# Optimization experiments

Measured on AMD Instinct MI355X. Metric: run time of the kernel, lower is better.

## Reference

```python
import jax, jax.numpy as jnp
import numpy as np

NUM_TREES = 256
DEPTH = 6
TREE_DIM = 2
INPUT_DIM = 256
BATCH = 2048


def sparsemax(x, axis=0):
    # Euclidean projection onto the simplex along `axis`.
    x = jnp.moveaxis(x, axis, -1)
    z = jnp.flip(jnp.sort(x, axis=-1), axis=-1)           # descending
    cz = jnp.cumsum(z, axis=-1)
    k = jnp.arange(1, x.shape[-1] + 1, dtype=x.dtype)
    support = (1.0 + k * z) > cz                          # boolean support set
    k_sel = jnp.sum(support, axis=-1, keepdims=True)      # |S(z)|
    tau = (jnp.take_along_axis(cz, k_sel - 1, axis=-1) - 1.0) / k_sel.astype(x.dtype)
    out = jnp.maximum(x - tau, 0.0)
    return jnp.moveaxis(out, -1, axis)


def sparsemoid(x):
    return jnp.clip(0.5 * x + 0.5, 0.0, 1.0)


def make_bin_codes(depth):
    idx = np.arange(2 ** depth)
    offs = 2 ** np.arange(depth)
    bc = ((idx[None, :] // offs[:, None]) % 2).astype(np.float32)  # [depth, 2^depth]
    return jnp.asarray(np.stack([bc, 1.0 - bc], axis=-1))          # [depth, 2^depth, 2]


def setup_inputs() -> dict:
    key = jax.random.key(0)
    ks = jax.random.split(key, 5)
    return {
        "inputs": jax.random.normal(ks[0], (BATCH, INPUT_DIM), dtype=jnp.float32),
        "feature_selection_logits": jax.random.normal(ks[1], (INPUT_DIM, NUM_TREES, DEPTH), dtype=jnp.float32),
        "feature_thresholds": jax.random.normal(ks[2], (NUM_TREES, DEPTH), dtype=jnp.float32) * 0.5,
        "log_temperatures": jax.random.normal(ks[3], (NUM_TREES, DEPTH), dtype=jnp.float32) * 0.1,
        "response": jax.random.normal(ks[4], (NUM_TREES, TREE_DIM, 2 ** DEPTH), dtype=jnp.float32),
    }


def reference(inputs, feature_selection_logits, feature_thresholds, log_temperatures, response):
    bin_codes_1hot = make_bin_codes(DEPTH)                                  # [d, 2^d, 2]
    selectors = sparsemax(feature_selection_logits, axis=0)                 # [i, n, d]
    feature_values = jnp.einsum('bi,ind->bnd', inputs, selectors)           # [b, n, d]
    tl = (feature_values - feature_thresholds) * jnp.exp(-log_temperatures) # [b, n, d]
    threshold_logits = jnp.stack([-tl, tl], axis=-1)                        # [b, n, d, 2]
    bins = sparsemoid(threshold_logits)                                     # [b, n, d, 2]
    bin_matches = jnp.einsum('bnds,dcs->bndc', bins, bin_codes_1hot)        # [b, n, d, 2^d]
    response_weights = jnp.prod(bin_matches, axis=-2)                       # [b, n, 2^d]
    out = jnp.einsum('bnc,ntc->bnt', response_weights, response)            # [b, n, tree_dim]
    return out.reshape(out.shape[0], -1)                                    # [b, n*tree_dim]
```

## Files before the change

kernel.cpp:

```cpp
#include <hip/hip_runtime.h>
#include <hip/hip_fp16.h>
#include <math.h>

#define NUM_TREES 256
#define DEPTH 6
#define TREE_DIM 2
#define INPUT_DIM 256
#define BATCH 2048
#define NLEAF 64
#define NCOLS (NUM_TREES * DEPTH)
#define KDIM INPUT_DIM

typedef _Float16 half8 __attribute__((ext_vector_type(8)));
typedef float floatx4 __attribute__((ext_vector_type(4)));

__global__ __launch_bounds__(256) void sparsemax_bisect(
    const float* __restrict__ fsl,
    const float* __restrict__ inputs,
    _Float16* __restrict__ selT,
    _Float16* __restrict__ inH)
{
    const int tid = threadIdx.x;
    {
        const int gid = blockIdx.x * 256 + tid;
        if (gid < (BATCH * INPUT_DIM) / 8) {
            const float4 v0 = ((const float4*)inputs)[gid * 2];
            const float4 v1 = ((const float4*)inputs)[gid * 2 + 1];
            half8 h;
            h[0] = (_Float16)v0.x; h[1] = (_Float16)v0.y;
            h[2] = (_Float16)v0.z; h[3] = (_Float16)v0.w;
            h[4] = (_Float16)v1.x; h[5] = (_Float16)v1.y;
            h[6] = (_Float16)v1.z; h[7] = (_Float16)v1.w;
            *(half8*)(inH + gid * 8) = h;
        }
    }

    const int lane = tid & 63;
    const int wave = tid >> 6;
    const int col  = blockIdx.x * 4 + wave;
    const int n = col / 6;
    const int d = col - n * 6;

    float x[4];
#pragma unroll
    for (int j = 0; j < 4; ++j)
        x[j] = fsl[(j * 64 + lane) * NCOLS + col];

    float mx = fmaxf(fmaxf(x[0], x[1]), fmaxf(x[2], x[3]));
#pragma unroll
    for (int off = 32; off > 0; off >>= 1)
        mx = fmaxf(mx, __shfl_xor(mx, off));

    float lo = mx - 1.0f, hi = mx;
    for (int it = 0; it < 16; ++it) {
        const float mid = 0.5f * (lo + hi);
        float s = fmaxf(x[0] - mid, 0.0f) + fmaxf(x[1] - mid, 0.0f)
                + fmaxf(x[2] - mid, 0.0f) + fmaxf(x[3] - mid, 0.0f);
#pragma unroll
        for (int off = 32; off > 0; off >>= 1)
            s += __shfl_xor(s, off);
        if (s > 1.0f) lo = mid; else hi = mid;
    }
    const float tau = 0.5f * (lo + hi);

    _Float16* dst = selT + (n * 8 + d) * KDIM;
#pragma unroll
    for (int j = 0; j < 4; ++j)
        dst[j * 64 + lane] = (_Float16)fmaxf(x[j] - tau, 0.0f);
}

#define BM 64
#define BN 64
#define BK 64
#define AP 72
#define BP 72
#define FVS 67
#define OSP 36

__global__ __launch_bounds__(256, 4) void odt_mfma_kernel(
    const _Float16* __restrict__ inH,
    const _Float16* __restrict__ selT,
    const float* __restrict__ thr,
    const float* __restrict__ logt,
    const float* __restrict__ resp,
    float* __restrict__ out)
{
    __shared__ union {
        struct {
            _Float16 A[BM][AP];
            _Float16 B[BN][BP];
        } s;
        float fv[BM][FVS];
    } u;
    __shared__ float respS[8 * TREE_DIM * NLEAF];
    __shared__ float outS[BM][OSP];

    const int tid = threadIdx.x;
    const int b0 = blockIdx.x * BM;
    const int treeBase = blockIdx.y * 8;
    const int colBase  = blockIdx.y * BN;

    ((float4*)respS)[tid] = ((const float4*)(resp + treeBase * TREE_DIM * NLEAF))[tid];

    const int lane = tid & 63;
    const int w    = tid >> 6;
    const int wm   = w >> 1, wn = w & 1;
    const int l16  = lane & 15, quad = lane >> 4;

    floatx4 acc[2][2];
#pragma unroll
    for (int mt = 0; mt < 2; ++mt)
#pragma unroll
        for (int nt = 0; nt < 2; ++nt)
            acc[mt][nt] = (floatx4){0.f, 0.f, 0.f, 0.f};

    const int srow = tid >> 2, sseg = tid & 3;
    const _Float16* aBase = inH  + (b0 + srow) * KDIM + sseg * 16;
    const _Float16* bBase = selT + (colBase + srow) * KDIM + sseg * 16;

    half8 pa0 = *(const half8*)(aBase);
    half8 pa1 = *(const half8*)(aBase + 8);
    half8 pb0 = *(const half8*)(bBase);
    half8 pb1 = *(const half8*)(bBase + 8);

#pragma unroll
    for (int k0 = 0; k0 < KDIM; k0 += BK) {
        __syncthreads();
        *(half8*)&u.s.A[srow][sseg * 16 + 0] = pa0;
        *(half8*)&u.s.A[srow][sseg * 16 + 8] = pa1;
        *(half8*)&u.s.B[srow][sseg * 16 + 0] = pb0;
        *(half8*)&u.s.B[srow][sseg * 16 + 8] = pb1;
        if (k0 + BK < KDIM) {
            pa0 = *(const half8*)(aBase + k0 + BK);
            pa1 = *(const half8*)(aBase + k0 + BK + 8);
            pb0 = *(const half8*)(bBase + k0 + BK);
            pb1 = *(const half8*)(bBase + k0 + BK + 8);
        }
        __syncthreads();

#pragma unroll
        for (int h = 0; h < 2; ++h) {
            const half8 bf0 = *(const half8*)&u.s.B[wn * 32 + l16][quad * 8 + h * 32];
            const half8 bf1 = *(const half8*)&u.s.B[wn * 32 + 16 + l16][quad * 8 + h * 32];
            const half8 af0 = *(const half8*)&u.s.A[wm * 32 + l16][quad * 8 + h * 32];
            const half8 af1 = *(const half8*)&u.s.A[wm * 32 + 16 + l16][quad * 8 + h * 32];
            acc[0][0] = __builtin_amdgcn_mfma_f32_16x16x32_f16(af0, bf0, acc[0][0], 0, 0, 0);
            acc[0][1] = __builtin_amdgcn_mfma_f32_16x16x32_f16(af0, bf1, acc[0][1], 0, 0, 0);
            acc[1][0] = __builtin_amdgcn_mfma_f32_16x16x32_f16(af1, bf0, acc[1][0], 0, 0, 0);
            acc[1][1] = __builtin_amdgcn_mfma_f32_16x16x32_f16(af1, bf1, acc[1][1], 0, 0, 0);
        }
    }

    __syncthreads();

#pragma unroll
    for (int mt = 0; mt < 2; ++mt)
#pragma unroll
        for (int nt = 0; nt < 2; ++nt)
#pragma unroll
            for (int r = 0; r < 4; ++r)
                u.fv[wm * 32 + mt * 16 + quad * 4 + r][wn * 32 + nt * 16 + l16] = acc[mt][nt][r];
    __syncthreads();

#pragma unroll
    for (int p = 0; p < 2; ++p) {
        const int idx = tid + 256 * p;
        const int row = idx & 63;
        const int tl  = idx >> 6;
        const int n   = treeBase + tl;
        const float* f = &u.fv[row][tl * 8];

        float sd[DEPTH];
#pragma unroll
        for (int d = 0; d < DEPTH; ++d) {
            const float tlg = (f[d] - thr[n * DEPTH + d]) * __expf(-logt[n * DEPTH + d]);
            sd[d] = fminf(fmaxf(0.5f + 0.5f * tlg, 0.0f), 1.0f);
        }
        float wv[NLEAF / 2];
        wv[0] = 1.0f;
#pragma unroll
        for (int d = 0; d < 5; ++d) {
            const int sz = 1 << d;
#pragma unroll
            for (int c2 = 0; c2 < 16; ++c2) {
                if (c2 < sz) {
                    const float t = wv[c2];
                    wv[c2]      = t * sd[d];
                    wv[c2 + sz] = t * (1.0f - sd[d]);
                }
            }
        }
        const float* r0 = &respS[tl * TREE_DIM * NLEAF];
        float a0 = 0.f, c0 = 0.f, a1 = 0.f, c1 = 0.f;
#pragma unroll
        for (int c2 = 0; c2 < 32; ++c2) {
            a0 = fmaf(wv[c2], r0[c2], a0);
            c0 = fmaf(wv[c2], r0[c2 + 32], c0);
            a1 = fmaf(wv[c2], r0[NLEAF + c2], a1);
            c1 = fmaf(wv[c2], r0[NLEAF + c2 + 32], c1);
        }
        const float s5 = sd[5], s5b = 1.0f - sd[5];
        float2 o;
        o.x = s5 * a0 + s5b * c0;
        o.y = s5 * a1 + s5b * c1;
        *(float2*)&outS[row][tl * 2] = o;
    }
    __syncthreads();

    {
        const int wrow = tid >> 2, wc = tid & 3;
        const float4 v = *(const float4*)&outS[wrow][wc * 4];
        *(float4*)(out + (b0 + wrow) * (NUM_TREES * TREE_DIM) + treeBase * 2 + wc * 4) = v;
    }
}

extern "C" void kernel_launch(void* const* d_in, const int* in_sizes, int n_in,
                              void* d_out, int out_size, void* d_ws, size_t ws_size,
                              hipStream_t stream) {
    const float* inputs = (const float*)d_in[0];
    const float* fsl    = (const float*)d_in[1];
    const float* thr    = (const float*)d_in[2];
    const float* logt   = (const float*)d_in[3];
    const float* resp   = (const float*)d_in[4];
    float* out = (float*)d_out;
    _Float16* selT = (_Float16*)d_ws;
    _Float16* inH  = (_Float16*)((char*)d_ws + (1 << 20));

    hipLaunchKernelGGL(sparsemax_bisect, dim3(NCOLS / 4), dim3(256), 0, stream,
                       fsl, inputs, selT, inH);
    hipLaunchKernelGGL(odt_mfma_kernel, dim3(BATCH / BM, NUM_TREES / 8), dim3(256),
                       0, stream, inH, selT, thr, logt, resp, out);
}
```

Baseline: 89.29 us.

## Quaternary-search sparsemax with exact tau, precompute threshold affine, pack responses

Replaces the 16-step bisection with a 6-step quaternary search plus an exact closed-form tau from the support set, which cuts the number of serial wave reductions. The first kernel also precomputes a per-column scale and offset from the thresholds and temperatures, so the main kernel applies one fma instead of an exp and two global loads. The response table is stored in shared memory as interleaved float4 so the leaf accumulation can use packed float2 FMAs. This adds a workspace buffer, and the exact tau depends on the support count from the coarse search being correct.

After: 86.41 us. -3.2%, faster.

```diff
diff --git a/kernel.cpp b/kernel.cpp
--- a/kernel.cpp
+++ b/kernel.cpp
@@ -13,12 +13,16 @@
 
 typedef _Float16 half8 __attribute__((ext_vector_type(8)));
 typedef float floatx4 __attribute__((ext_vector_type(4)));
+typedef float floatx2 __attribute__((ext_vector_type(2)));
 
 __global__ __launch_bounds__(256) void sparsemax_bisect(
     const float* __restrict__ fsl,
     const float* __restrict__ inputs,
+    const float* __restrict__ thr,
+    const float* __restrict__ logt,
     _Float16* __restrict__ selT,
-    _Float16* __restrict__ inH)
+    _Float16* __restrict__ inH,
+    float2* __restrict__ ab)
 {
     const int tid = threadIdx.x;
     {
@@ -52,21 +56,54 @@
         mx = fmaxf(mx, __shfl_xor(mx, off));
 
     float lo = mx - 1.0f, hi = mx;
-    for (int it = 0; it < 16; ++it) {
-        const float mid = 0.5f * (lo + hi);
-        float s = fmaxf(x[0] - mid, 0.0f) + fmaxf(x[1] - mid, 0.0f)
-                + fmaxf(x[2] - mid, 0.0f) + fmaxf(x[3] - mid, 0.0f);
-#pragma unroll
-        for (int off = 32; off > 0; off >>= 1)
-            s += __shfl_xor(s, off);
-        if (s > 1.0f) lo = mid; else hi = mid;
-    }
-    const float tau = 0.5f * (lo + hi);
+#pragma unroll
+    for (int it = 0; it < 6; ++it) {
+        const float w  = hi - lo;
+        const float m1 = lo + 0.25f * w;
+        const float m2 = lo + 0.50f * w;
+        const float m3 = lo + 0.75f * w;
+        float s1 = 0.f, s2 = 0.f, s3 = 0.f;
+#pragma unroll
+        for (int j = 0; j < 4; ++j) {
+            s1 += fmaxf(x[j] - m1, 0.0f);
+            s2 += fmaxf(x[j] - m2, 0.0f);
+            s3 += fmaxf(x[j] - m3, 0.0f);
+        }
+#pragma unroll
+        for (int off = 32; off > 0; off >>= 1) {
+            s1 += __shfl_xor(s1, off);
+            s2 += __shfl_xor(s2, off);
+            s3 += __shfl_xor(s3, off);
+        }
+        lo = (s3 > 1.0f) ? m3 : (s2 > 1.0f) ? m2 : (s1 > 1.0f) ? m1 : lo;
+        hi = (s1 <= 1.0f) ? m1 : (s2 <= 1.0f) ? m2 : (s3 <= 1.0f) ? m3 : hi;
+    }
+
+    const float mid = 0.5f * (lo + hi);
+    float ssum = 0.f, scnt = 0.f;
+#pragma unroll
+    for (int j = 0; j < 4; ++j) {
+        const bool in = x[j] > mid;
+        ssum += in ? x[j] : 0.0f;
+        scnt += in ? 1.0f : 0.0f;
+    }
+#pragma unroll
+    for (int off = 32; off > 0; off >>= 1) {
+        ssum += __shfl_xor(ssum, off);
+        scnt += __shfl_xor(scnt, off);
+    }
+    const float tau = (ssum - 1.0f) / scnt;
 
     _Float16* dst = selT + (n * 8 + d) * KDIM;
 #pragma unroll
     for (int j = 0; j < 4; ++j)
         dst[j * 64 + lane] = (_Float16)fmaxf(x[j] - tau, 0.0f);
+
+    if (lane == 0) {
+        const float sa = 0.5f * __expf(-logt[col]);
+        const float sb = 0.5f - sa * thr[col];
+        ab[col] = make_float2(sa, sb);
+    }
 }
 
 #define BM 64
@@ -80,8 +117,7 @@
 __global__ __launch_bounds__(256, 4) void odt_mfma_kernel(
     const _Float16* __restrict__ inH,
     const _Float16* __restrict__ selT,
-    const float* __restrict__ thr,
-    const float* __restrict__ logt,
+    const float2* __restrict__ ab,
     const float* __restrict__ resp,
     float* __restrict__ out)
 {
@@ -92,7 +128,8 @@
         } s;
         float fv[BM][FVS];
     } u;
-    __shared__ float respS[8 * TREE_DIM * NLEAF];
+    __shared__ float4 respP[8][32];
+    __shared__ float2 abS[48];
     __shared__ float outS[BM][OSP];
 
     const int tid = threadIdx.x;
@@ -100,7 +137,12 @@
     const int treeBase = blockIdx.y * 8;
     const int colBase  = blockIdx.y * BN;
 
-    ((float4*)respS)[tid] = ((const float4*)(resp + treeBase * TREE_DIM * NLEAF))[tid];
+    {
+        const int tr = tid >> 5, c2 = tid & 31;
+        const float* rb = resp + (treeBase + tr) * (TREE_DIM * NLEAF);
+        respP[tr][c2] = make_float4(rb[c2], rb[32 + c2], rb[64 + c2], rb[96 + c2]);
+        if (tid < 48) abS[tid] = ab[treeBase * DEPTH + tid];
+    }
 
     const int lane = tid & 63;
     const int w    = tid >> 6;
@@ -167,15 +209,14 @@
         const int idx = tid + 256 * p;
         const int row = idx & 63;
         const int tl  = idx >> 6;
-        const int n   = treeBase + tl;
         const float* f = &u.fv[row][tl * 8];
+        const float2* abt = &abS[tl * DEPTH];
 
         float sd[DEPTH];
 #pragma unroll
-        for (int d = 0; d < DEPTH; ++d) {
-            const float tlg = (f[d] - thr[n * DEPTH + d]) * __expf(-logt[n * DEPTH + d]);
-            sd[d] = fminf(fmaxf(0.5f + 0.5f * tlg, 0.0f), 1.0f);
-        }
+        for (int d = 0; d < DEPTH; ++d)
+            sd[d] = fminf(fmaxf(fmaf(f[d], abt[d].x, abt[d].y), 0.0f), 1.0f);
+
         float wv[NLEAF / 2];
         wv[0] = 1.0f;
 #pragma unroll
@@ -190,19 +231,20 @@
                 }
             }
         }
-        const float* r0 = &respS[tl * TREE_DIM * NLEAF];
-        float a0 = 0.f, c0 = 0.f, a1 = 0.f, c1 = 0.f;
+        const float4* rp = &respP[tl][0];
+        floatx2 A0 = (floatx2){0.f, 0.f};
+        floatx2 A1 = (floatx2){0.f, 0.f};
 #pragma unroll
         for (int c2 = 0; c2 < 32; ++c2) {
-            a0 = fmaf(wv[c2], r0[c2], a0);
-            c0 = fmaf(wv[c2], r0[c2 + 32], c0);
-            a1 = fmaf(wv[c2], r0[NLEAF + c2], a1);
-            c1 = fmaf(wv[c2], r0[NLEAF + c2 + 32], c1);
+            const float4 rr = rp[c2];
+            const floatx2 w2 = (floatx2){wv[c2], wv[c2]};
+            A0 = w2 * (floatx2){rr.x, rr.y} + A0;
+            A1 = w2 * (floatx2){rr.z, rr.w} + A1;
         }
         const float s5 = sd[5], s5b = 1.0f - sd[5];
         float2 o;
-        o.x = s5 * a0 + s5b * c0;
-        o.y = s5 * a1 + s5b * c1;
+        o.x = s5 * A0[0] + s5b * A0[1];
+        o.y = s5 * A1[0] + s5b * A1[1];
         *(float2*)&outS[row][tl * 2] = o;
     }
     __syncthreads();
@@ -225,9 +267,10 @@
     float* out = (float*)d_out;
     _Float16* selT = (_Float16*)d_ws;
     _Float16* inH  = (_Float16*)((char*)d_ws + (1 << 20));
+    float2*   ab   = (float2*)((char*)d_ws + (2 << 20));
 
     hipLaunchKernelGGL(sparsemax_bisect, dim3(NCOLS / 4), dim3(256), 0, stream,
-                       fsl, inputs, selT, inH);
+                       fsl, inputs, thr, logt, selT, inH, ab);
     hipLaunchKernelGGL(odt_mfma_kernel, dim3(BATCH / BM, NUM_TREES / 8), dim3(256),
-                       0, stream, inH, selT, thr, logt, resp, out);
+                       0, stream, inH, selT, ab, resp, out);
 }
```
